# Optimization experiments

Measured on AMD Instinct MI355X. Metric: run time of the kernel, lower is better.

Reference implementation:

```python
import jax, jax.numpy as jnp
import numpy as np

# dims: batch, seqlen, d_model, d_inner=2*d_model, d_state, dt_rank=ceil(dm/16), n_layer, vocab, d_conv
B_, L_, DM, DI, N, RK, NL, V, K = 2, 2048, 512, 1024, 16, 32, 4, 32000, 4


def setup_inputs() -> dict:
    key = jax.random.key(0)
    ks = jax.random.split(key, 10)
    s = lambda k, shape, scale: jax.random.normal(k, shape, jnp.float32) * scale
    return {
        "input_ids": jax.random.randint(ks[0], (B_, L_), 0, V),
        "emb": s(ks[1], (V, DM), 0.02),
        "in_proj_w": s(ks[2], (NL, 2 * DI, DM), DM ** -0.5),
        "conv_w": s(ks[3], (NL, DI, K), 0.2),
        "conv_b": jnp.zeros((NL, DI), jnp.float32),
        "x_proj_w": s(ks[4], (NL, RK + 2 * N, DI), DI ** -0.5),
        "dt_proj_w": s(ks[5], (NL, DI, RK), RK ** -0.5),
        "dt_proj_b": jnp.full((NL, DI), -4.6, jnp.float32),  # softplus^-1(~0.01)
        "A_log": jnp.tile(jnp.log(jnp.arange(1, N + 1, dtype=jnp.float32))[None, None, :], (NL, DI, 1)),
        "Dp": jnp.ones((NL, DI), jnp.float32),
        "out_proj_w": s(ks[6], (NL, DM, DI), DI ** -0.5),
        "norm_w": jnp.ones((NL, DM), jnp.float32),
        "norm_b": jnp.zeros((NL, DM), jnp.float32),
        "normf_w": jnp.ones((DM,), jnp.float32),
        "normf_b": jnp.zeros((DM,), jnp.float32),
        "dec_w": s(ks[7], (V, DM), DM ** -0.5),
        "dec_b": jnp.zeros((V,), jnp.float32),
    }


def layer_norm(x, w, b, eps=1e-5):
    m = x.mean(-1, keepdims=True)
    v = ((x - m) ** 2).mean(-1, keepdims=True)
    return (x - m) * jax.lax.rsqrt(v + eps) * w + b


def mamba_mixer(x, iw, cw, cb, xw, dw, db, A_log, Dv, ow):
    B, L, _ = x.shape
    xz = x @ iw.T                      # [B,L,2*DI]
    u, z = jnp.split(xz, 2, -1)
    # depthwise causal conv1d, kernel K
    up = jnp.pad(u, ((0, 0), (K - 1, 0), (0, 0)))
    u = sum(up[:, k:k + L, :] * cw[:, k] for k in range(K)) + cb
    u = jax.nn.silu(u)
    xdbl = u @ xw.T                    # [B,L,RK+2N]
    dt, Bm, Cm = jnp.split(xdbl, [RK, RK + N], -1)
    dt = jax.nn.softplus(dt @ dw.T + db)   # [B,L,DI]
    A = -jnp.exp(A_log)                    # [DI,N]
    dA = jnp.exp(dt[..., None] * A)                              # [B,L,DI,N]
    dBu = dt[..., None] * Bm[:, :, None, :] * u[..., None]       # [B,L,DI,N]

    def step(h, inp):
        dA_t, dBu_t, C_t = inp
        h = dA_t * h + dBu_t
        return h, jnp.einsum('bdn,bn->bd', h, C_t)

    h0 = jnp.zeros((B, DI, N), x.dtype)
    _, ys = jax.lax.scan(step, h0, (dA.transpose(1, 0, 2, 3), dBu.transpose(1, 0, 2, 3), Cm.transpose(1, 0, 2)))
    y = ys.transpose(1, 0, 2) + u * Dv
    y = y * jax.nn.silu(z)
    return y @ ow.T


def reference(input_ids, emb, in_proj_w, conv_w, conv_b, x_proj_w, dt_proj_w, dt_proj_b,
              A_log, Dp, out_proj_w, norm_w, norm_b, normf_w, normf_b, dec_w, dec_b):
    h = emb[input_ids]                 # [B,L,DM]
    residual = None
    for i in range(NL):
        residual = h + residual if residual is not None else h
        hn = layer_norm(residual, norm_w[i], norm_b[i])
        h = mamba_mixer(hn, in_proj_w[i], conv_w[i], conv_b[i], x_proj_w[i],
                        dt_proj_w[i], dt_proj_b[i], A_log[i], Dp[i], out_proj_w[i])
    residual = h + residual
    h = layer_norm(residual, normf_w, normf_b)
    return h @ dec_w.T + dec_b         # [B,L,V]
```

## Files before the change

kernel.cpp:

```cpp
#include <hip/hip_runtime.h>
#include <cstdint>
#include <cstddef>

typedef unsigned short u16;
typedef __attribute__((ext_vector_type(8))) short short8;
typedef __attribute__((ext_vector_type(4))) float f32x4;
typedef __attribute__((ext_vector_type(4))) unsigned short us4;

#define NB 2
#define SEQ 2048
#define DMODEL 512
#define DINNER 1024
#define NSTATE 16
#define RKK 32
#define NLAYER 4
#define VOCAB 32000
#define MROWS 4096
#define NCHUNK 64
#define LCHUNK 32
#define XP_SPLITK 8
#define XP_KCH 128
#define OUT_SPLITK 4

#define GLOAD16(gp, lp) __builtin_amdgcn_global_load_lds( \
    (const __attribute__((address_space(1))) void*)(gp),  \
    (__attribute__((address_space(3))) void*)(lp), 16, 0, 0)

static __device__ __forceinline__ u16 f2bf(float f) {
  union { float f; uint32_t u; } v; v.f = f;
  uint32_t r = (v.u + 0x7FFFu + ((v.u >> 16) & 1u)) >> 16;
  return (u16)r;
}
static __device__ __forceinline__ float bf2f(u16 x) {
  union { uint32_t u; float f; } v; v.u = ((uint32_t)x) << 16; return v.f;
}

__global__ __launch_bounds__(256) void cvt_all_k(
    const float* __restrict__ ipw, const float* __restrict__ dtw,
    const float* __restrict__ opw, const float* __restrict__ dw,
    const float* __restrict__ xpw,
    u16* __restrict__ w_in, u16* __restrict__ w_dt,
    u16* __restrict__ w_out, u16* __restrict__ w_dec,
    u16* __restrict__ w_xp) {
  const long n0 = (long)NLAYER * 2 * DINNER * DMODEL / 4;
  const long n1 = (long)NLAYER * DINNER * RKK / 4;
  const long n2 = (long)NLAYER * DMODEL * DINNER / 4;
  const long n3 = (long)VOCAB * DMODEL / 4;
  const long n4 = (long)NLAYER * 128 * DINNER / 4;
  long i = (long)blockIdx.x * 256 + threadIdx.x;
  if (i >= n0 + n1 + n2 + n3 + n4) return;
  if (i >= n0 + n1 + n2 + n3) {
    long o4 = (i - n0 - n1 - n2 - n3) * 4;
    int c = (int)(o4 & 1023); int r = ((int)(o4 >> 10)) & 127; int l = (int)(o4 >> 17);
    us4 o;
    if (r < 64) {
      f32x4 v = *(const f32x4*)(xpw + (((long)l * 64 + r) << 10) + c);
      o.x = f2bf(v.x); o.y = f2bf(v.y); o.z = f2bf(v.z); o.w = f2bf(v.w);
    } else { o.x = 0; o.y = 0; o.z = 0; o.w = 0; }
    *(us4*)(w_xp + o4) = o;
    return;
  }
  const float* s; u16* d; long off;
  if (i < n0) { s = ipw; d = w_in; off = i; }
  else if (i < n0 + n1) { s = dtw; d = w_dt; off = i - n0; }
  else if (i < n0 + n1 + n2) { s = opw; d = w_out; off = i - n0 - n1; }
  else { s = dw; d = w_dec; off = i - n0 - n1 - n2; }
  f32x4 v = *(const f32x4*)(s + off * 4);
  us4 o; o.x = f2bf(v.x); o.y = f2bf(v.y); o.z = f2bf(v.z); o.w = f2bf(v.w);
  *(us4*)(d + off * 4) = o;
}

template <int MODE>
__global__ __launch_bounds__(256) void ln_k(const int* __restrict__ ids, const float* __restrict__ emb,
                                            float* __restrict__ resid, const float* __restrict__ hP,
                                            long pstride,
                                            const float* __restrict__ w, const float* __restrict__ b,
                                            u16* __restrict__ obf) {
  int m = blockIdx.x, t = threadIdx.x;
  long base = (long)m * DMODEL;
  float x0, x1;
  if (MODE == 0) {
    long ebase = (long)ids[m] * DMODEL;
    x0 = emb[ebase + t]; x1 = emb[ebase + t + 256];
    resid[base + t] = x0; resid[base + t + 256] = x1;
  } else {
    x0 = resid[base + t];
    x1 = resid[base + t + 256];
    #pragma unroll
    for (int z = 0; z < OUT_SPLITK; ++z) {
      x0 += hP[z * pstride + base + t];
      x1 += hP[z * pstride + base + t + 256];
    }
    resid[base + t] = x0; resid[base + t + 256] = x1;
  }
  float s = x0 + x1, q = x0 * x0 + x1 * x1;
  #pragma unroll
  for (int o = 1; o < 64; o <<= 1) { s += __shfl_xor(s, o, 64); q += __shfl_xor(q, o, 64); }
  __shared__ float ss[4], qq[4];
  int wv = t >> 6;
  if ((t & 63) == 0) { ss[wv] = s; qq[wv] = q; }
  __syncthreads();
  s = ss[0] + ss[1] + ss[2] + ss[3];
  q = qq[0] + qq[1] + qq[2] + qq[3];
  float mean = s * (1.f / DMODEL);
  float var = q * (1.f / DMODEL) - mean * mean;
  float rs = rsqrtf(var + 1e-5f);
  obf[base + t]       = f2bf((x0 - mean) * rs * w[t] + b[t]);
  obf[base + t + 256] = f2bf((x1 - mean) * rs * w[t + 256] + b[t + 256]);
}

__global__ __launch_bounds__(256) void conv_silu_k(const u16* __restrict__ xzb, const float* __restrict__ cw,
                            const float* __restrict__ cb, u16* __restrict__ ub) {
  int tid = blockIdx.x * 256 + threadIdx.x;
  int d = tid & (DINNER - 1);
  int g = tid >> 10;
  int m0 = g << 3;
  int t0 = m0 & (SEQ - 1);
  float w0 = cw[d * 4 + 0], w1 = cw[d * 4 + 1], w2 = cw[d * 4 + 2], w3 = cw[d * 4 + 3];
  float bias = cb[d];
  float v[11];
  #pragma unroll
  for (int j = 0; j < 11; ++j) {
    int tt = t0 + j - 3;
    v[j] = (tt >= 0) ? bf2f(xzb[(long)(m0 + j - 3) * (2 * DINNER) + d]) : 0.f;
  }
  #pragma unroll
  for (int i = 0; i < 8; ++i) {
    float acc = bias + v[i] * w0 + v[i + 1] * w1 + v[i + 2] * w2 + v[i + 3] * w3;
    float sv = acc / (1.f + __expf(-acc));
    ub[(long)(m0 + i) * DINNER + d] = f2bf(sv);
  }
}

template <int EPI, int BK, bool SPLIT>
__global__ __launch_bounds__(256) void gemm_bf16(
    const u16* __restrict__ A, int lda, const u16* __restrict__ W, int ldw,
    float* __restrict__ C, u16* __restrict__ Cb, int ldc,
    const float* __restrict__ bias, int K, int kchunk, long zstride) {
  const int tid = threadIdx.x;
  const int nwg = gridDim.x * gridDim.y;
  const int wgid = blockIdx.y * gridDim.x + blockIdx.x;
  const int q = nwg >> 3;
  const int swz = (wgid & 7) * q + (wgid >> 3);
  const int bn = swz % gridDim.x, bm = swz / gridDim.x;
  int kb = 0, ke = K;
  if (SPLIT) { kb = blockIdx.z * kchunk; ke = kb + kchunk; C += (long)blockIdx.z * zstride; }
  const int wave = tid >> 6, lane = tid & 63;
  const int wm = (wave >> 1) * 64, wn = (wave & 1) * 64;
  __shared__ __align__(16) u16 sA[128 * BK];
  __shared__ __align__(16) u16 sB[128 * BK];
  f32x4 acc[4][4] = {};
  const long arow0 = (long)bm * 128, brow0 = (long)bn * 128;
  const int frow = lane & 15, fk = (lane >> 4) << 3;
  const int rsw = (frow & 7) << 3;
  for (int k0 = kb; k0 < ke; k0 += BK) {
    __syncthreads();
    if (BK == 32) {
      const int srow = lane >> 2, scol = (lane & 3) << 3;
      #pragma unroll
      for (int i = 0; i < 2; ++i) {
        int c = wave * 2 + i;
        GLOAD16(A + (arow0 + 16 * c + srow) * (long)lda + k0 + scol, sA + c * 512);
        GLOAD16(W + (brow0 + 16 * c + srow) * (long)ldw + k0 + scol, sB + c * 512);
      }
    } else {
      const int srow = lane >> 3;
      const int scol = (((lane & 7) ^ (lane >> 3)) << 3);
      #pragma unroll
      for (int i = 0; i < 4; ++i) {
        int c = wave * 4 + i;
        GLOAD16(A + (arow0 + 8 * c + srow) * (long)lda + k0 + scol, sA + c * 512);
        GLOAD16(W + (brow0 + 8 * c + srow) * (long)ldw + k0 + scol, sB + c * 512);
      }
    }
    asm volatile("s_waitcnt vmcnt(0)" ::: "memory");
    __syncthreads();
    #pragma unroll
    for (int ks = 0; ks < BK / 32; ++ks) {
      short8 aF[4], bF[4];
      #pragma unroll
      for (int i = 0; i < 4; ++i) {
        int idx = (wm + i * 16 + frow) * BK + ks * 32 + fk;
        aF[i] = *(const short8*)(sA + (BK == 64 ? (idx ^ rsw) : idx));
      }
      #pragma unroll
      for (int i = 0; i < 4; ++i) {
        int idx = (wn + i * 16 + frow) * BK + ks * 32 + fk;
        bF[i] = *(const short8*)(sB + (BK == 64 ? (idx ^ rsw) : idx));
      }
      #pragma unroll
      for (int mi = 0; mi < 4; ++mi)
        #pragma unroll
        for (int ni = 0; ni < 4; ++ni)
          acc[mi][ni] = __builtin_amdgcn_mfma_f32_16x16x32_bf16(aF[mi], bF[ni], acc[mi][ni], 0, 0, 0);
    }
  }
  const int ccol = lane & 15, crow = (lane >> 4) << 2;
  #pragma unroll
  for (int mi = 0; mi < 4; ++mi) {
    #pragma unroll
    for (int ni = 0; ni < 4; ++ni) {
      long gr0 = arow0 + wm + mi * 16 + crow;
      long gc = brow0 + wn + ni * 16 + ccol;
      #pragma unroll
      for (int r = 0; r < 4; ++r) {
        float v = acc[mi][ni][r];
        long idx = (gr0 + r) * (long)ldc + gc;
        if (EPI == 0) {
          C[idx] = v;
        } else if (EPI == 1) {
          Cb[idx] = f2bf(v);
        } else if (EPI == 2) {
          float x = v + bias[gc];
          Cb[idx] = f2bf((x > 20.f) ? x : log1pf(__expf(x)));
        } else {
          __builtin_nontemporal_store(v + bias[gc], &C[idx]);
        }
      }
    }
  }
}

__global__ __launch_bounds__(512) void gemm_dec(
    const u16* __restrict__ A, const u16* __restrict__ W,
    float* __restrict__ C, const float* __restrict__ bias) {
  const int tid = threadIdx.x;
  const int nwg = gridDim.x * gridDim.y;
  const int wgid = blockIdx.y * gridDim.x + blockIdx.x;
  const int q = nwg >> 3;
  const int swz = (wgid & 7) * q + (wgid >> 3);
  const int bn = swz % gridDim.x, bm = swz / gridDim.x;
  const int wave = tid >> 6, lane = tid & 63;
  const int wm = (wave >> 1) << 6;
  const int wn = (wave & 1) << 6;
  __shared__ __align__(16) u16 sA[2][256 * 32];
  __shared__ __align__(16) u16 sB[2][128 * 32];
  f32x4 acc[4][4] = {};
  const long arow0 = (long)bm * 256, brow0 = (long)bn * 128;
  const int frow = lane & 15, fk = (lane >> 4) << 3;
  const int srow = lane >> 2;
  const int scol = (((lane & 3) ^ (srow & 3)) << 3);
  #pragma unroll
  for (int i = 0; i < 2; ++i) {
    int c = wave * 2 + i;
    GLOAD16(A + (arow0 + 16 * c + srow) * (long)DMODEL + scol, sA[0] + c * 512);
  }
  GLOAD16(W + (brow0 + 16 * wave + srow) * (long)DMODEL + scol, sB[0] + wave * 512);
  asm volatile("s_waitcnt vmcnt(0)" ::: "memory");
  __syncthreads();
  int cur = 0;
  for (int k0 = 0; k0 < DMODEL; k0 += 32) {
    if (k0 + 32 < DMODEL) {
      int nb = cur ^ 1;
      #pragma unroll
      for (int i = 0; i < 2; ++i) {
        int c = wave * 2 + i;
        GLOAD16(A + (arow0 + 16 * c + srow) * (long)DMODEL + k0 + 32 + scol, sA[nb] + c * 512);
      }
      GLOAD16(W + (brow0 + 16 * wave + srow) * (long)DMODEL + k0 + 32 + scol, sB[nb] + wave * 512);
    }
    short8 aF[4], bF[4];
    #pragma unroll
    for (int i = 0; i < 4; ++i) {
      int row = wm + i * 16 + frow;
      aF[i] = *(const short8*)(sA[cur] + ((row * 32 + fk) ^ ((row & 3) << 3)));
    }
    #pragma unroll
    for (int i = 0; i < 4; ++i) {
      int row = wn + i * 16 + frow;
      bF[i] = *(const short8*)(sB[cur] + ((row * 32 + fk) ^ ((row & 3) << 3)));
    }
    #pragma unroll
    for (int mi = 0; mi < 4; ++mi)
      #pragma unroll
      for (int ni = 0; ni < 4; ++ni)
        acc[mi][ni] = __builtin_amdgcn_mfma_f32_16x16x32_bf16(aF[mi], bF[ni], acc[mi][ni], 0, 0, 0);
    asm volatile("s_waitcnt vmcnt(0)" ::: "memory");
    __syncthreads();
    cur ^= 1;
  }
  const int ccol = lane & 15, crow = (lane >> 4) << 2;
  #pragma unroll
  for (int mi = 0; mi < 4; ++mi) {
    #pragma unroll
    for (int ni = 0; ni < 4; ++ni) {
      long gr0 = arow0 + wm + mi * 16 + crow;
      long gc = brow0 + wn + ni * 16 + ccol;
      float bv = bias[gc];
      #pragma unroll
      for (int r = 0; r < 4; ++r)
        __builtin_nontemporal_store(acc[mi][ni][r] + bv, &C[(gr0 + r) * (long)VOCAB + gc]);
    }
  }
}

__global__ __launch_bounds__(256) void xp_comb_k(const float* __restrict__ P, float* __restrict__ xd,
                          u16* __restrict__ xdb) {
  long i = (long)blockIdx.x * 256 + threadIdx.x;
  int col = (int)(i & 127);
  if (col >= 64) return;
  float s = 0.f;
  #pragma unroll
  for (int z = 0; z < XP_SPLITK; ++z) s += P[(long)z * MROWS * 128 + i];
  if (col < 32) xdb[i] = f2bf(s);
  else xd[i] = s;
}

__global__ __launch_bounds__(256) void scanA_k(const u16* __restrict__ dtb, const u16* __restrict__ ubf,
                        const float* __restrict__ xd, const float* __restrict__ alog_l,
                        float* __restrict__ P, float* __restrict__ S) {
  int bid = blockIdx.x;
  int tid = threadIdx.x;
  int b = bid >> 8;
  int c = (bid >> 2) & (NCHUNK - 1);
  int d = ((bid & 3) << 8) + tid;
  long rbase = (long)(b * SEQ + c * LCHUNK);
  __shared__ __align__(16) float sB[LCHUNK][NSTATE];
  if (tid < 128) {
    int t = tid >> 2, k4 = (tid & 3) << 2;
    *(f32x4*)&sB[t][k4] = *(const f32x4*)(xd + (rbase + t) * 128 + RKK + k4);
  }
  u16 dtv[LCHUNK], uv[LCHUNK];
  const u16* dp = dtb + rbase * DINNER + d;
  const u16* up = ubf + rbase * DINNER + d;
  #pragma unroll
  for (int tt = 0; tt < LCHUNK; ++tt) { dtv[tt] = dp[(long)tt * DINNER]; uv[tt] = up[(long)tt * DINNER]; }
  float A[NSTATE], h[NSTATE];
  #pragma unroll
  for (int n4 = 0; n4 < 4; ++n4) {
    f32x4 a4 = *(const f32x4*)(alog_l + d * NSTATE + n4 * 4);
    #pragma unroll
    for (int j = 0; j < 4; ++j) { A[n4 * 4 + j] = -__expf(a4[j]); h[n4 * 4 + j] = 0.f; }
  }
  __syncthreads();
  float dsum = 0.f;
  #pragma unroll
  for (int tt = 0; tt < LCHUNK; ++tt) {
    float dv = bf2f(dtv[tt]);
    float du = dv * bf2f(uv[tt]);
    dsum += dv;
    f32x4 b0 = *(const f32x4*)&sB[tt][0], b1 = *(const f32x4*)&sB[tt][4];
    f32x4 b2 = *(const f32x4*)&sB[tt][8], b3 = *(const f32x4*)&sB[tt][12];
    #pragma unroll
    for (int n = 0; n < NSTATE; ++n) {
      float dA = __expf(dv * A[n]);
      float bx = (n < 4) ? b0[n & 3] : (n < 8) ? b1[n & 3] : (n < 12) ? b2[n & 3] : b3[n & 3];
      h[n] = dA * h[n] + du * bx;
    }
  }
  long base = (((long)(b * DINNER + d)) * NCHUNK + c) * NSTATE;
  #pragma unroll
  for (int n4 = 0; n4 < 4; ++n4) {
    f32x4 pv, sv;
    #pragma unroll
    for (int j = 0; j < 4; ++j) { pv[j] = __expf(A[n4 * 4 + j] * dsum); sv[j] = h[n4 * 4 + j]; }
    *(f32x4*)(P + base + n4 * 4) = pv;
    *(f32x4*)(S + base + n4 * 4) = sv;
  }
}

__global__ __launch_bounds__(256) void scanB_k(const float* __restrict__ P, const float* __restrict__ S,
                        float* __restrict__ Hin) {
  int w = blockIdx.x * 4 + (threadIdx.x >> 6);
  int lane = threadIdx.x & 63;
  long base = ((long)w * NCHUNK + lane) * NSTATE;
  float p[NSTATE], s[NSTATE];
  #pragma unroll
  for (int n = 0; n < NSTATE; ++n) { p[n] = P[base + n]; s[n] = S[base + n]; }
  #pragma unroll
  for (int off = 1; off < 64; off <<= 1) {
    float pp[NSTATE], sp[NSTATE];
    #pragma unroll
    for (int n = 0; n < NSTATE; ++n) {
      pp[n] = __shfl_up(p[n], off, 64);
      sp[n] = __shfl_up(s[n], off, 64);
    }
    if (lane >= off) {
      #pragma unroll
      for (int n = 0; n < NSTATE; ++n) { s[n] = p[n] * sp[n] + s[n]; p[n] *= pp[n]; }
    }
  }
  #pragma unroll
  for (int n = 0; n < NSTATE; ++n) {
    float hv = __shfl_up(s[n], 1, 64);
    Hin[base + n] = (lane == 0) ? 0.f : hv;
  }
}

__global__ __launch_bounds__(256) void scanC_k(const u16* __restrict__ dtb, const u16* __restrict__ ubf,
                        const float* __restrict__ xd, const float* __restrict__ alog_l,
                        const float* __restrict__ Dp_l, const u16* __restrict__ xzb,
                        const float* __restrict__ Hin, u16* __restrict__ ybf) {
  int bid = blockIdx.x;
  int tid = threadIdx.x;
  int b = bid >> 8;
  int c = (bid >> 2) & (NCHUNK - 1);
  int d = ((bid & 3) << 8) + tid;
  long rbase = (long)(b * SEQ + c * LCHUNK);
  __shared__ __align__(16) float sBC[LCHUNK][2 * NSTATE];
  {
    int t = tid >> 3, k4 = (tid & 7) << 2;
    *(f32x4*)&sBC[t][k4] = *(const f32x4*)(xd + (rbase + t) * 128 + RKK + k4);
  }
  u16 dtv[LCHUNK], uv[LCHUNK], zv[LCHUNK];
  const u16* dp = dtb + rbase * DINNER + d;
  const u16* up = ubf + rbase * DINNER + d;
  const u16* zp = xzb + rbase * (2 * DINNER) + DINNER + d;
  #pragma unroll
  for (int tt = 0; tt < LCHUNK; ++tt) {
    dtv[tt] = dp[(long)tt * DINNER]; uv[tt] = up[(long)tt * DINNER];
    zv[tt] = zp[(long)tt * 2 * DINNER];
  }
  float A[NSTATE], h[NSTATE];
  long hbase = (((long)(b * DINNER + d)) * NCHUNK + c) * NSTATE;
  #pragma unroll
  for (int n4 = 0; n4 < 4; ++n4) {
    f32x4 a4 = *(const f32x4*)(alog_l + d * NSTATE + n4 * 4);
    f32x4 h4 = *(const f32x4*)(Hin + hbase + n4 * 4);
    #pragma unroll
    for (int j = 0; j < 4; ++j) { A[n4 * 4 + j] = -__expf(a4[j]); h[n4 * 4 + j] = h4[j]; }
  }
  float Dv = Dp_l[d];
  u16* yp = ybf + rbase * DINNER + d;
  __syncthreads();
  #pragma unroll
  for (int tt = 0; tt < LCHUNK; ++tt) {
    float dv = bf2f(dtv[tt]);
    float uvf = bf2f(uv[tt]);
    float du = dv * uvf;
    f32x4 b0 = *(const f32x4*)&sBC[tt][0], b1 = *(const f32x4*)&sBC[tt][4];
    f32x4 b2 = *(const f32x4*)&sBC[tt][8], b3 = *(const f32x4*)&sBC[tt][12];
    f32x4 c0 = *(const f32x4*)&sBC[tt][16], c1 = *(const f32x4*)&sBC[tt][20];
    f32x4 c2 = *(const f32x4*)&sBC[tt][24], c3 = *(const f32x4*)&sBC[tt][28];
    float y = 0.f;
    #pragma unroll
    for (int n = 0; n < NSTATE; ++n) {
      float dA = __expf(dv * A[n]);
      float bx = (n < 4) ? b0[n & 3] : (n < 8) ? b1[n & 3] : (n < 12) ? b2[n & 3] : b3[n & 3];
      float cx = (n < 4) ? c0[n & 3] : (n < 8) ? c1[n & 3] : (n < 12) ? c2[n & 3] : c3[n & 3];
      h[n] = dA * h[n] + du * bx;
      y += h[n] * cx;
    }
    y += uvf * Dv;
    float z = bf2f(zv[tt]);
    y *= z / (1.f + __expf(-z));
    yp[(long)tt * DINNER] = f2bf(y);
  }
}

extern "C" void kernel_launch(void* const* d_in, const int* in_sizes, int n_in,
                              void* d_out, int out_size, void* d_ws, size_t ws_size,
                              hipStream_t stream) {
  (void)in_sizes; (void)n_in; (void)out_size; (void)ws_size;
  const int*   ids = (const int*)d_in[0];
  const float* emb = (const float*)d_in[1];
  const float* ipw = (const float*)d_in[2];
  const float* cw  = (const float*)d_in[3];
  const float* cb  = (const float*)d_in[4];
  const float* xpw = (const float*)d_in[5];
  const float* dtw = (const float*)d_in[6];
  const float* dtb = (const float*)d_in[7];
  const float* alg = (const float*)d_in[8];
  const float* Dpp = (const float*)d_in[9];
  const float* opw = (const float*)d_in[10];
  const float* nw  = (const float*)d_in[11];
  const float* nb  = (const float*)d_in[12];
  const float* nfw = (const float*)d_in[13];
  const float* nfb = (const float*)d_in[14];
  const float* dw  = (const float*)d_in[15];
  const float* db  = (const float*)d_in[16];

  char* p = (char*)d_ws;
  auto carve = [&](size_t bytes) { void* r = (void*)p; p += (bytes + 255) & ~(size_t)255; return r; };
  float* resid  = (float*)carve((size_t)MROWS * DMODEL * 4);
  float* hmixP  = (float*)carve((size_t)OUT_SPLITK * MROWS * DMODEL * 4);
  u16*   hnbf   = (u16*)  carve((size_t)MROWS * DMODEL * 2);
  u16*   hfbf   = (u16*)  carve((size_t)MROWS * DMODEL * 2);
  u16*   xzb    = (u16*)  carve((size_t)MROWS * 2 * DINNER * 2);
  u16*   ubf    = (u16*)  carve((size_t)MROWS * DINNER * 2);
  float* xdbl   = (float*)carve((size_t)MROWS * 128 * 4);
  u16*   xdblbf = (u16*)  carve((size_t)MROWS * 128 * 2);
  float* xdP    = (float*)carve((size_t)XP_SPLITK * MROWS * 128 * 4);
  u16*   dtb16  = (u16*)  carve((size_t)MROWS * DINNER * 2);
  u16*   ybf    = (u16*)  carve((size_t)MROWS * DINNER * 2);
  float* chkP   = (float*)carve((size_t)NB * DINNER * NCHUNK * NSTATE * 4);
  float* chkS   = (float*)carve((size_t)NB * DINNER * NCHUNK * NSTATE * 4);
  float* hin    = (float*)carve((size_t)NB * DINNER * NCHUNK * NSTATE * 4);
  u16*   w_in   = (u16*)carve((size_t)NLAYER * 2 * DINNER * DMODEL * 2);
  u16*   w_xp   = (u16*)carve((size_t)NLAYER * 128 * DINNER * 2);
  u16*   w_dt   = (u16*)carve((size_t)NLAYER * DINNER * RKK * 2);
  u16*   w_out  = (u16*)carve((size_t)NLAYER * DMODEL * DINNER * 2);
  u16*   w_dec  = (u16*)carve((size_t)VOCAB * DMODEL * 2);

  {
    long nv = ((long)NLAYER * 2 * DINNER * DMODEL + (long)NLAYER * DINNER * RKK +
               (long)NLAYER * DMODEL * DINNER + (long)VOCAB * DMODEL +
               (long)NLAYER * 128 * DINNER) / 4;
    cvt_all_k<<<(int)((nv + 255) / 256), 256, 0, stream>>>(
        ipw, dtw, opw, dw, xpw, w_in, w_dt, w_out, w_dec, w_xp);
  }

  for (int i = 0; i < NLAYER; ++i) {
    if (i == 0)
      ln_k<0><<<MROWS, 256, 0, stream>>>(ids, emb, resid, nullptr, 0, nw, nb, hnbf);
    else
      ln_k<1><<<MROWS, 256, 0, stream>>>(nullptr, nullptr, resid, hmixP, (long)MROWS * DMODEL,
                                         nw + i * DMODEL, nb + i * DMODEL, hnbf);
    gemm_bf16<1, 64, false><<<dim3(2 * DINNER / 128, MROWS / 128), 256, 0, stream>>>(
        hnbf, DMODEL, w_in + (long)i * 2 * DINNER * DMODEL, DMODEL,
        nullptr, xzb, 2 * DINNER, nullptr, DMODEL, 0, 0);
    conv_silu_k<<<(MROWS / 8 * DINNER) / 256, 256, 0, stream>>>(
        xzb, cw + (long)i * DINNER * 4, cb + i * DINNER, ubf);
    gemm_bf16<0, 64, true><<<dim3(1, MROWS / 128, XP_SPLITK), 256, 0, stream>>>(
        ubf, DINNER, w_xp + (long)i * 128 * DINNER, DINNER,
        xdP, nullptr, 128, nullptr, DINNER, XP_KCH, (long)MROWS * 128);
    xp_comb_k<<<(MROWS * 128) / 256, 256, 0, stream>>>(xdP, xdbl, xdblbf);
    gemm_bf16<2, 32, false><<<dim3(DINNER / 128, MROWS / 128), 256, 0, stream>>>(
        xdblbf, 128, w_dt + (long)i * DINNER * RKK, RKK,
        nullptr, dtb16, DINNER, dtb + i * DINNER, RKK, 0, 0);
    scanA_k<<<NB * NCHUNK * 4, 256, 0, stream>>>(
        dtb16, ubf, xdbl, alg + (long)i * DINNER * NSTATE, chkP, chkS);
    scanB_k<<<(NB * DINNER) / 4, 256, 0, stream>>>(chkP, chkS, hin);
    scanC_k<<<NB * NCHUNK * 4, 256, 0, stream>>>(
        dtb16, ubf, xdbl, alg + (long)i * DINNER * NSTATE, Dpp + i * DINNER, xzb, hin, ybf);
    gemm_bf16<0, 64, true><<<dim3(DMODEL / 128, MROWS / 128, OUT_SPLITK), 256, 0, stream>>>(
        ybf, DINNER, w_out + (long)i * DMODEL * DINNER, DINNER,
        hmixP, nullptr, DMODEL, nullptr, DINNER, DINNER / OUT_SPLITK, (long)MROWS * DMODEL);
  }
  ln_k<1><<<MROWS, 256, 0, stream>>>(nullptr, nullptr, resid, hmixP, (long)MROWS * DMODEL,
                                     nfw, nfb, hfbf);
  gemm_dec<<<dim3(VOCAB / 128, MROWS / 256), 512, 0, stream>>>(
      hfbf, w_dec, (float*)d_out, db);
}
```

Before: 774.6 us.

## Enlarge decoder GEMM tile to 256x256 with 64-wide K stages

The vocabulary-projection GEMM now uses a 256x256 output tile per workgroup instead of 256x128, with each wave owning a 128x64 sub-tile. The K step grows from 32 to 64 with an 8-row XOR LDS swizzle, and loads run two stages ahead using partial vmcnt waits. The aim is to halve activation re-reads across the vocab dimension and to amortise barriers over more MFMAs per step. In exchange it uses 128KB of LDS and 128 accumulator floats per thread, which limits occupancy to one workgroup per CU and risks register pressure or spills under the launch-bounds hint.

```diff
diff --git a/kernel.cpp b/kernel.cpp
--- a/kernel.cpp
+++ b/kernel.cpp
@@ -221,7 +221,7 @@
   }
 }
 
-__global__ __launch_bounds__(512) void gemm_dec(
+__global__ __launch_bounds__(512, 2) void gemm_dec(
     const u16* __restrict__ A, const u16* __restrict__ W,
     float* __restrict__ C, const float* __restrict__ bias) {
   const int tid = threadIdx.x;
@@ -231,65 +231,72 @@
   const int swz = (wgid & 7) * q + (wgid >> 3);
   const int bn = swz % gridDim.x, bm = swz / gridDim.x;
   const int wave = tid >> 6, lane = tid & 63;
-  const int wm = (wave >> 1) << 6;
-  const int wn = (wave & 1) << 6;
-  __shared__ __align__(16) u16 sA[2][256 * 32];
-  __shared__ __align__(16) u16 sB[2][128 * 32];
-  f32x4 acc[4][4] = {};
-  const long arow0 = (long)bm * 256, brow0 = (long)bn * 128;
+  const int wm = (wave >> 2) << 7;
+  const int wn = (wave & 3) << 6;
+  __shared__ __align__(16) u16 sA[2][256 * 64];
+  __shared__ __align__(16) u16 sB[2][256 * 64];
+  f32x4 acc[8][4] = {};
+  const long arow0 = (long)bm * 256, brow0 = (long)bn * 256;
   const int frow = lane & 15, fk = (lane >> 4) << 3;
-  const int srow = lane >> 2;
-  const int scol = (((lane & 3) ^ (srow & 3)) << 3);
-  #pragma unroll
-  for (int i = 0; i < 2; ++i) {
-    int c = wave * 2 + i;
-    GLOAD16(A + (arow0 + 16 * c + srow) * (long)DMODEL + scol, sA[0] + c * 512);
-  }
-  GLOAD16(W + (brow0 + 16 * wave + srow) * (long)DMODEL + scol, sB[0] + wave * 512);
-  asm volatile("s_waitcnt vmcnt(0)" ::: "memory");
+  const int rsw = (frow & 7) << 3;
+  const int srow = lane >> 3;
+  const int scol = (((lane & 7) ^ (lane >> 3)) << 3);
+  const int NT = DMODEL / 64;
+  #define DEC_STAGE(b, kt) do {                                                     \
+    int k0 = (kt) * 64;                                                             \
+    _Pragma("unroll")                                                               \
+    for (int i = 0; i < 4; ++i) {                                                   \
+      int c = wave * 4 + i;                                                         \
+      GLOAD16(A + (arow0 + 8 * c + srow) * (long)DMODEL + k0 + scol, sA[b] + c * 512); \
+      GLOAD16(W + (brow0 + 8 * c + srow) * (long)DMODEL + k0 + scol, sB[b] + c * 512); \
+    }                                                                               \
+  } while (0)
+  DEC_STAGE(0, 0);
+  DEC_STAGE(1, 1);
+  asm volatile("s_waitcnt vmcnt(8)" ::: "memory");
   __syncthreads();
-  int cur = 0;
-  for (int k0 = 0; k0 < DMODEL; k0 += 32) {
-    if (k0 + 32 < DMODEL) {
-      int nb = cur ^ 1;
-      #pragma unroll
-      for (int i = 0; i < 2; ++i) {
-        int c = wave * 2 + i;
-        GLOAD16(A + (arow0 + 16 * c + srow) * (long)DMODEL + k0 + 32 + scol, sA[nb] + c * 512);
-      }
-      GLOAD16(W + (brow0 + 16 * wave + srow) * (long)DMODEL + k0 + 32 + scol, sB[nb] + wave * 512);
-    }
-    short8 aF[4], bF[4];
-    #pragma unroll
-    for (int i = 0; i < 4; ++i) {
-      int row = wm + i * 16 + frow;
-      aF[i] = *(const short8*)(sA[cur] + ((row * 32 + fk) ^ ((row & 3) << 3)));
-    }
-    #pragma unroll
-    for (int i = 0; i < 4; ++i) {
-      int row = wn + i * 16 + frow;
-      bF[i] = *(const short8*)(sB[cur] + ((row * 32 + fk) ^ ((row & 3) << 3)));
-    }
-    #pragma unroll
-    for (int mi = 0; mi < 4; ++mi)
-      #pragma unroll
-      for (int ni = 0; ni < 4; ++ni)
-        acc[mi][ni] = __builtin_amdgcn_mfma_f32_16x16x32_bf16(aF[mi], bF[ni], acc[mi][ni], 0, 0, 0);
-    asm volatile("s_waitcnt vmcnt(0)" ::: "memory");
+  for (int kt = 0; kt < NT; ++kt) {
+    const int cb = kt & 1;
+    #pragma unroll
+    for (int ks = 0; ks < 2; ++ks) {
+      short8 aF[8], bF[4];
+      #pragma unroll
+      for (int i = 0; i < 8; ++i) {
+        int row = wm + i * 16 + frow;
+        aF[i] = *(const short8*)(sA[cb] + ((row * 64 + ks * 32 + fk) ^ rsw));
+      }
+      #pragma unroll
+      for (int j = 0; j < 4; ++j) {
+        int row = wn + j * 16 + frow;
+        bF[j] = *(const short8*)(sB[cb] + ((row * 64 + ks * 32 + fk) ^ rsw));
+      }
+      #pragma unroll
+      for (int i = 0; i < 8; ++i)
+        #pragma unroll
+        for (int j = 0; j < 4; ++j)
+          acc[i][j] = __builtin_amdgcn_mfma_f32_16x16x32_bf16(aF[i], bF[j], acc[i][j], 0, 0, 0);
+    }
     __syncthreads();
-    cur ^= 1;
-  }
+    if (kt + 2 < NT) {
+      DEC_STAGE(cb, kt + 2);
+      asm volatile("s_waitcnt vmcnt(8)" ::: "memory");
+    } else {
+      asm volatile("s_waitcnt vmcnt(0)" ::: "memory");
+    }
+    __syncthreads();
+  }
+  #undef DEC_STAGE
   const int ccol = lane & 15, crow = (lane >> 4) << 2;
   #pragma unroll
-  for (int mi = 0; mi < 4; ++mi) {
-    #pragma unroll
-    for (int ni = 0; ni < 4; ++ni) {
-      long gr0 = arow0 + wm + mi * 16 + crow;
-      long gc = brow0 + wn + ni * 16 + ccol;
+  for (int i = 0; i < 8; ++i) {
+    #pragma unroll
+    for (int j = 0; j < 4; ++j) {
+      long gr0 = arow0 + wm + i * 16 + crow;
+      long gc = brow0 + wn + j * 16 + ccol;
       float bv = bias[gc];
       #pragma unroll
       for (int r = 0; r < 4; ++r)
-        __builtin_nontemporal_store(acc[mi][ni][r] + bv, &C[(gr0 + r) * (long)VOCAB + gc]);
+        __builtin_nontemporal_store(acc[i][j][r] + bv, &C[(gr0 + r) * (long)VOCAB + gc]);
     }
   }
 }
@@ -529,6 +536,6 @@
   }
   ln_k<1><<<MROWS, 256, 0, stream>>>(nullptr, nullptr, resid, hmixP, (long)MROWS * DMODEL,
                                      nfw, nfb, hfbf);
-  gemm_dec<<<dim3(VOCAB / 128, MROWS / 256), 512, 0, stream>>>(
+  gemm_dec<<<dim3(VOCAB / 256, MROWS / 256), 512, 0, stream>>>(
       hfbf, w_dec, (float*)d_out, db);
 }
```

Result: slower. 794.6 us (+2.6%).
